# Kernel tuning notes

Measured on AMD Instinct MI355X. Metric: run time of the kernel, lower is better.

## Reference

```python
import jax, jax.numpy as jnp
import numpy as np

N = 100000   # nodes
E = 1200000  # edges
IN, HID, OUT = 64, 64, 64
G = 64       # graphs in the batch


def setup_inputs() -> dict:
    key = jax.random.key(0)
    ks = jax.random.split(key, 7)
    x = jax.random.normal(ks[0], (N, IN), dtype=jnp.float32)
    edge_index = jax.random.randint(ks[1], (2, E), 0, N, dtype=jnp.int32)
    batch = jnp.sort(jax.random.randint(ks[2], (N,), 0, G, dtype=jnp.int32))
    W1 = jax.random.normal(ks[3], (IN, HID), dtype=jnp.float32) * (1.0 / np.sqrt(IN))
    b1 = jnp.zeros((HID,), dtype=jnp.float32)
    W2 = jax.random.normal(ks[4], (HID, OUT), dtype=jnp.float32) * (1.0 / np.sqrt(HID))
    b2 = jnp.zeros((OUT,), dtype=jnp.float32)
    return {"x": x, "edge_index": edge_index, "batch": batch,
            "W1": W1, "b1": b1, "W2": W2, "b2": b2}


def _gcn_conv(x, W, b, src, dst, dinv):
    # x' = D^{-1/2} (A + I) D^{-1/2} (x W) + b   (PyG GCNConv with self-loops)
    h = x @ W                                   # [N, F_out]
    norm = dinv[src] * dinv[dst]                # [E]
    agg = jax.ops.segment_sum(h[src] * norm[:, None], dst, num_segments=N)
    agg = agg + h * (dinv * dinv)[:, None]      # self-loop contribution
    return agg + b


def reference(x, edge_index, batch, W1, b1, W2, b2):
    src, dst = edge_index[0], edge_index[1]
    # degree with self-loops, counted at the aggregation target (PyG convention)
    deg = jax.ops.segment_sum(jnp.ones((E,), x.dtype), dst, num_segments=N) + 1.0
    dinv = jax.lax.rsqrt(deg)

    h1 = jax.nn.relu(_gcn_conv(x, W1, b1, src, dst, dinv))   # [N, HID]
    s1 = jax.ops.segment_sum(h1, batch, num_segments=G)      # [G, HID]
    h2 = jax.nn.relu(_gcn_conv(h1, W2, b2, src, dst, dinv))  # [N, OUT]
    s2 = jax.ops.segment_sum(h2, batch, num_segments=G)      # [G, OUT]
    return h2, jnp.concatenate([s1, s2], axis=1)
```

## Files before the change

kernel.cpp:

```cpp
#include <hip/hip_runtime.h>


#define FDIM 64
#define BSHIFT 7
#define MAXNB 1024
#define EBCAP 2048
#define COLCAP 3072
#define BCAP 4096

__device__ __forceinline__ unsigned short f2bf(float f) {
    union { float f; unsigned int u; } a; a.f = f;
    unsigned int u = a.u;
    unsigned int r = u + 0x7fffu + ((u >> 16) & 1u);
    return (unsigned short)(r >> 16);
}
__device__ __forceinline__ float bf2f(unsigned short s) {
    union { unsigned int u; float f; } a; a.u = ((unsigned int)s) << 16;
    return a.f;
}

__global__ __launch_bounds__(256, 4) void k_pre(
    const int* __restrict__ src, const int* __restrict__ dstp, int E,
    const int* __restrict__ batch, int N, int G, int gemmB, int scatB,
    const float* __restrict__ x, const float* __restrict__ W1,
    int* __restrict__ bucketFill, int* __restrict__ gstart,
    unsigned short* __restrict__ gb1, unsigned int* __restrict__ ebuf) {
    __shared__ __align__(16) char sm[33792];
    int tid = threadIdx.x;
    int bx = blockIdx.x;
    if (bx < gemmB) {
        float4* Ws = (float4*)sm;
        float (*Xs)[68] = (float(*)[68])(sm + 16384);
        ushort4* GB4 = (ushort4*)gb1;
        if (bx == 0 && tid < 16) GB4[(size_t)N * 16 + tid] = make_ushort4(0, 0, 0, 0);
        const float4* W4 = (const float4*)W1;
        for (int i = tid; i < 1024; i += 256) Ws[i] = W4[i];
        int rowBase = bx * 64;
        for (int i = tid; i < 1024; i += 256) {
            int r = i >> 4, f4 = i & 15;
            float4 v = make_float4(0.f, 0.f, 0.f, 0.f);
            if (rowBase + r < N) v = ((const float4*)x)[(size_t)(rowBase + r) * 16 + f4];
            *(float4*)&Xs[r][f4 * 4] = v;
        }
        __syncthreads();
        int r0 = (tid >> 4) * 4;
        int c4 = tid & 15;
        float4 acc0 = make_float4(0,0,0,0), acc1 = acc0, acc2 = acc0, acc3 = acc0;
#pragma unroll 16
        for (int k = 0; k < 64; k++) {
            float4 w = Ws[k * 16 + c4];
            float x0 = Xs[r0 + 0][k], x1 = Xs[r0 + 1][k], x2 = Xs[r0 + 2][k], x3 = Xs[r0 + 3][k];
            acc0.x += x0 * w.x; acc0.y += x0 * w.y; acc0.z += x0 * w.z; acc0.w += x0 * w.w;
            acc1.x += x1 * w.x; acc1.y += x1 * w.y; acc1.z += x1 * w.z; acc1.w += x1 * w.w;
            acc2.x += x2 * w.x; acc2.y += x2 * w.y; acc2.z += x2 * w.z; acc2.w += x2 * w.w;
            acc3.x += x3 * w.x; acc3.y += x3 * w.y; acc3.z += x3 * w.z; acc3.w += x3 * w.w;
        }
        float4 a[4] = {acc0, acc1, acc2, acc3};
#pragma unroll
        for (int i = 0; i < 4; i++) {
            int row = rowBase + r0 + i;
            if (row < N) {
                ushort4 pk;
                pk.x = f2bf(a[i].x); pk.y = f2bf(a[i].y);
                pk.z = f2bf(a[i].z); pk.w = f2bf(a[i].w);
                GB4[(size_t)row * 16 + c4] = pk;
            }
        }
        return;
    }
    if (bx < gemmB + scatB) {
        int* hist = (int*)sm;
        int* base = hist + MAXNB;
        for (int i = tid; i < MAXNB; i += 256) hist[i] = 0;
        __syncthreads();
        int e0 = (bx - gemmB) * 4096;
        int s[16], d[16], r[16];
#pragma unroll
        for (int k = 0; k < 16; k++) {
            int e = e0 + k * 256 + tid;
            bool valid = e < E;
            s[k] = valid ? src[e] : 0;
            d[k] = valid ? dstp[e] : 0;
            r[k] = valid ? atomicAdd(&hist[d[k] >> BSHIFT], 1) : 0;
        }
        __syncthreads();
        for (int i = tid; i < MAXNB; i += 256) {
            int c = hist[i];
            base[i] = c ? (i << 11) + atomicAdd(&bucketFill[i], c) : 0;
        }
        __syncthreads();
#pragma unroll
        for (int k = 0; k < 16; k++) {
            int e = e0 + k * 256 + tid;
            if (e < E)
                ebuf[base[d[k] >> BSHIFT] + r[k]] =
                    (unsigned int)s[k] | ((unsigned int)(d[k] & 127) << 17);
        }
        return;
    }
    int i = (bx - gemmB - scatB) * 256 + tid;
    if (i < N) {
        int b = batch[i];
        if (i == 0) { for (int g = 0; g <= b; g++) gstart[g] = 0; }
        else {
            int pp = batch[i - 1];
            for (int g = pp + 1; g <= b; g++) gstart[g] = i;
        }
        if (i == N - 1) { for (int g = b + 1; g <= G; g++) gstart[g] = N; }
    }
}

__global__ __launch_bounds__(256) void k_bsort(const unsigned int* __restrict__ ebuf,
                                               const int* __restrict__ bucketFill, int N,
                                               int* __restrict__ row_ptr,
                                               int* __restrict__ row_blocks,
                                               int* __restrict__ col,
                                               float* __restrict__ dinv,
                                               unsigned short* __restrict__ gb1) {
    __shared__ int cntL[128];
    __shared__ int scanL[128];
    __shared__ int fillL[128];
    __shared__ int colL[BCAP];
    __shared__ int padT;
    int b = blockIdx.x;
    int n0 = b << BSHIFT;
    int nCnt = N - n0; if (nCnt > 128) nCnt = 128;
    int t = threadIdx.x;
    if (b == 0 && t == 0) dinv[N] = 0.f;
    int cnt = bucketFill[b]; if (cnt > EBCAP) cnt = EBCAP;
    int lo = b << 11, hi = lo + cnt;
    int outBase = b * COLCAP;
    if (t < 128) { cntL[t] = 0; fillL[t] = 0; }
    __syncthreads();
    for (int e = lo + t; e < hi; e += 256)
        atomicAdd(&cntL[ebuf[e] >> 17], 1);
    __syncthreads();
    int pc = 0;
    if (t < 128) { pc = (cntL[t] + 7) & ~7; scanL[t] = pc; }
    __syncthreads();
    for (int off = 1; off < 128; off <<= 1) {
        int u = (t >= off && t < 128) ? scanL[t - off] : 0;
        __syncthreads();
        if (t < 128) scanL[t] += u;
        __syncthreads();
    }
    if (t == 127) padT = scanL[127];
    if (t < nCnt) {
        int ex = scanL[t] - pc;
        row_ptr[n0 + t] = outBase + ex;
        row_blocks[n0 + t] = pc >> 3;
        dinv[n0 + t] = rsqrtf((float)cntL[t] + 1.0f);
        scanL[t] = ex;
    }
    __syncthreads();
    int padTotal = padT;
    if (padTotal <= BCAP) {
        for (int i = t; i < padTotal; i += 256) colL[i] = N;
        __syncthreads();
        for (int e = lo + t; e < hi; e += 256) {
            unsigned int pr = ebuf[e];
            int d = pr >> 17;
            int r = scanL[d] + atomicAdd(&fillL[d], 1);
            colL[r] = (int)(pr & 0x1FFFFu);
        }
        __syncthreads();
        for (int i = t; i < padTotal; i += 256) col[outBase + i] = colL[i];
    } else {
        for (int e = lo + t; e < hi; e += 256) {
            unsigned int pr = ebuf[e];
            int d = pr >> 17;
            int r = scanL[d] + atomicAdd(&fillL[d], 1);
            col[outBase + r] = (int)(pr & 0x1FFFFu);
        }
        __syncthreads();
        if (t < nCnt) {
            int pcl = (cntL[t] + 7) & ~7;
            for (int i = cntL[t]; i < pcl; i++) col[outBase + scanL[t] + i] = N;
        }
    }
    __syncthreads();
    ushort4* GB4 = (ushort4*)gb1;
    for (int i = t; i < nCnt * 16; i += 256) {
        int row = i >> 4, u4 = i & 15;
        float dn = rsqrtf((float)cntL[row] + 1.0f);
        size_t idx = (size_t)(n0 + row) * 16 + u4;
        ushort4 u = GB4[idx];
        u.x = f2bf(bf2f(u.x) * dn);
        u.y = f2bf(bf2f(u.y) * dn);
        u.z = f2bf(bf2f(u.z) * dn);
        u.w = f2bf(bf2f(u.w) * dn);
        GB4[idx] = u;
    }
}

template <typename OutT>
__global__ __launch_bounds__(256) void k_agg(
    const unsigned short* __restrict__ Gb,
    const int* __restrict__ row_ptr, const int* __restrict__ row_blocks,
    const int* __restrict__ col, const float* __restrict__ dinv,
    const float* __restrict__ bias, int N, OutT* __restrict__ Out) {
    int w = threadIdx.x >> 6;
    int c = threadIdx.x & 63;
    int n = blockIdx.x * 4 + w;
    if (n >= N) return;
    int e = row_ptr[n];
    int nb8 = row_blocks[n];
    float acc = bf2f(Gb[(size_t)n * FDIM + c]);
    for (; nb8 >= 2; nb8 -= 2, e += 16) {
        int4 ca = *(const int4*)(col + e);
        int4 cb = *(const int4*)(col + e + 4);
        int4 cc = *(const int4*)(col + e + 8);
        int4 cd = *(const int4*)(col + e + 12);
        int s0  = __builtin_amdgcn_readfirstlane(ca.x);
        int s1  = __builtin_amdgcn_readfirstlane(ca.y);
        int s2  = __builtin_amdgcn_readfirstlane(ca.z);
        int s3  = __builtin_amdgcn_readfirstlane(ca.w);
        int s4  = __builtin_amdgcn_readfirstlane(cb.x);
        int s5  = __builtin_amdgcn_readfirstlane(cb.y);
        int s6  = __builtin_amdgcn_readfirstlane(cb.z);
        int s7  = __builtin_amdgcn_readfirstlane(cb.w);
        int s8  = __builtin_amdgcn_readfirstlane(cc.x);
        int s9  = __builtin_amdgcn_readfirstlane(cc.y);
        int s10 = __builtin_amdgcn_readfirstlane(cc.z);
        int s11 = __builtin_amdgcn_readfirstlane(cc.w);
        int s12 = __builtin_amdgcn_readfirstlane(cd.x);
        int s13 = __builtin_amdgcn_readfirstlane(cd.y);
        int s14 = __builtin_amdgcn_readfirstlane(cd.z);
        int s15 = __builtin_amdgcn_readfirstlane(cd.w);
        float a0  = bf2f(Gb[(size_t)s0  * FDIM + c]);
        float a1  = bf2f(Gb[(size_t)s1  * FDIM + c]);
        float a2  = bf2f(Gb[(size_t)s2  * FDIM + c]);
        float a3  = bf2f(Gb[(size_t)s3  * FDIM + c]);
        float a4  = bf2f(Gb[(size_t)s4  * FDIM + c]);
        float a5  = bf2f(Gb[(size_t)s5  * FDIM + c]);
        float a6  = bf2f(Gb[(size_t)s6  * FDIM + c]);
        float a7  = bf2f(Gb[(size_t)s7  * FDIM + c]);
        float a8  = bf2f(Gb[(size_t)s8  * FDIM + c]);
        float a9  = bf2f(Gb[(size_t)s9  * FDIM + c]);
        float a10 = bf2f(Gb[(size_t)s10 * FDIM + c]);
        float a11 = bf2f(Gb[(size_t)s11 * FDIM + c]);
        float a12 = bf2f(Gb[(size_t)s12 * FDIM + c]);
        float a13 = bf2f(Gb[(size_t)s13 * FDIM + c]);
        float a14 = bf2f(Gb[(size_t)s14 * FDIM + c]);
        float a15 = bf2f(Gb[(size_t)s15 * FDIM + c]);
        acc += (((a0 + a1) + (a2 + a3)) + ((a4 + a5) + (a6 + a7)))
             + (((a8 + a9) + (a10 + a11)) + ((a12 + a13) + (a14 + a15)));
    }
    if (nb8) {
        int4 ca = *(const int4*)(col + e);
        int4 cb = *(const int4*)(col + e + 4);
        int s0 = __builtin_amdgcn_readfirstlane(ca.x);
        int s1 = __builtin_amdgcn_readfirstlane(ca.y);
        int s2 = __builtin_amdgcn_readfirstlane(ca.z);
        int s3 = __builtin_amdgcn_readfirstlane(ca.w);
        int s4 = __builtin_amdgcn_readfirstlane(cb.x);
        int s5 = __builtin_amdgcn_readfirstlane(cb.y);
        int s6 = __builtin_amdgcn_readfirstlane(cb.z);
        int s7 = __builtin_amdgcn_readfirstlane(cb.w);
        float a0 = bf2f(Gb[(size_t)s0 * FDIM + c]);
        float a1 = bf2f(Gb[(size_t)s1 * FDIM + c]);
        float a2 = bf2f(Gb[(size_t)s2 * FDIM + c]);
        float a3 = bf2f(Gb[(size_t)s3 * FDIM + c]);
        float a4 = bf2f(Gb[(size_t)s4 * FDIM + c]);
        float a5 = bf2f(Gb[(size_t)s5 * FDIM + c]);
        float a6 = bf2f(Gb[(size_t)s6 * FDIM + c]);
        float a7 = bf2f(Gb[(size_t)s7 * FDIM + c]);
        acc += ((a0 + a1) + (a2 + a3)) + ((a4 + a5) + (a6 + a7));
    }
    float v = fmaxf(acc * dinv[n] + bias[c], 0.f);
    if constexpr (sizeof(OutT) == 2)
        Out[(size_t)n * FDIM + c] = f2bf(v);
    else
        Out[(size_t)n * FDIM + c] = v;
}

__global__ __launch_bounds__(256, 4) void k_gemm2(
    const unsigned short* __restrict__ H1b, const float* __restrict__ W2,
    const float* __restrict__ dinv, int N, unsigned short* __restrict__ Gb2) {
    __shared__ float4 Ws[64 * 16];
    __shared__ float Xs[64][68];
    int tid = threadIdx.x;
    ushort4* GB4 = (ushort4*)Gb2;
    if (blockIdx.x == 0 && tid < 16)
        GB4[(size_t)N * 16 + tid] = make_ushort4(0, 0, 0, 0);
    const float4* W4 = (const float4*)W2;
    for (int i = tid; i < 1024; i += 256) Ws[i] = W4[i];
    int rowBase = blockIdx.x * 64;
    const ushort4* H4 = (const ushort4*)H1b;
    for (int i = tid; i < 1024; i += 256) {
        int r = i >> 4, u4 = i & 15;
        float4 v = make_float4(0.f, 0.f, 0.f, 0.f);
        if (rowBase + r < N) {
            ushort4 u = H4[(size_t)(rowBase + r) * 16 + u4];
            v = make_float4(bf2f(u.x), bf2f(u.y), bf2f(u.z), bf2f(u.w));
        }
        *(float4*)&Xs[r][u4 * 4] = v;
    }
    __syncthreads();
    int r0 = (tid >> 4) * 4;
    int c4 = tid & 15;
    float4 acc0 = make_float4(0,0,0,0), acc1 = acc0, acc2 = acc0, acc3 = acc0;
#pragma unroll 16
    for (int k = 0; k < 64; k++) {
        float4 w = Ws[k * 16 + c4];
        float x0 = Xs[r0 + 0][k], x1 = Xs[r0 + 1][k], x2 = Xs[r0 + 2][k], x3 = Xs[r0 + 3][k];
        acc0.x += x0 * w.x; acc0.y += x0 * w.y; acc0.z += x0 * w.z; acc0.w += x0 * w.w;
        acc1.x += x1 * w.x; acc1.y += x1 * w.y; acc1.z += x1 * w.z; acc1.w += x1 * w.w;
        acc2.x += x2 * w.x; acc2.y += x2 * w.y; acc2.z += x2 * w.z; acc2.w += x2 * w.w;
        acc3.x += x3 * w.x; acc3.y += x3 * w.y; acc3.z += x3 * w.z; acc3.w += x3 * w.w;
    }
    float4 a[4] = {acc0, acc1, acc2, acc3};
#pragma unroll
    for (int i = 0; i < 4; i++) {
        int row = rowBase + r0 + i;
        if (row < N) {
            float dn = dinv[row];
            ushort4 pk;
            pk.x = f2bf(a[i].x * dn);
            pk.y = f2bf(a[i].y * dn);
            pk.z = f2bf(a[i].z * dn);
            pk.w = f2bf(a[i].w * dn);
            GB4[(size_t)row * 16 + c4] = pk;
        }
    }
}

__global__ __launch_bounds__(256) void k_pool(const unsigned short* __restrict__ H1b,
                                              const float4* __restrict__ H2,
                                              const int* __restrict__ gstart,
                                              float* __restrict__ pool) {
    int g = blockIdx.x & 63;
    int layer = blockIdx.x >> 6;
    int lo = gstart[g], hi = gstart[g + 1];
    int c4 = threadIdx.x & 15;
    int rl = threadIdx.x >> 4;
    float4 acc = make_float4(0.f, 0.f, 0.f, 0.f);
    if (layer == 0) {
        const ushort4* H = (const ushort4*)H1b;
        for (int r = lo + rl; r < hi; r += 16) {
            ushort4 u = H[(size_t)r * 16 + c4];
            acc.x += bf2f(u.x); acc.y += bf2f(u.y);
            acc.z += bf2f(u.z); acc.w += bf2f(u.w);
        }
    } else {
        for (int r = lo + rl; r < hi; r += 16) {
            float4 v = H2[(size_t)r * 16 + c4];
            acc.x += v.x; acc.y += v.y; acc.z += v.z; acc.w += v.w;
        }
    }
    __shared__ float4 sm[16][16];
    sm[rl][c4] = acc;
    __syncthreads();
    if (rl == 0) {
        float4 s = sm[0][c4];
#pragma unroll
        for (int k = 1; k < 16; k++) {
            float4 v = sm[k][c4];
            s.x += v.x; s.y += v.y; s.z += v.z; s.w += v.w;
        }
        float* dstq = &pool[(size_t)g * 128 + layer * 64 + c4 * 4];
        dstq[0] = s.x; dstq[1] = s.y; dstq[2] = s.z; dstq[3] = s.w;
    }
}

static inline size_t align256(size_t x) { return (x + 255) & ~(size_t)255; }

extern "C" void kernel_launch(void* const* d_in, const int* in_sizes, int n_in,
                              void* d_out, int out_size, void* d_ws, size_t ws_size,
                              hipStream_t stream) {
    const float* x     = (const float*)d_in[0];
    const int*   ei    = (const int*)d_in[1];
    const int*   batch = (const int*)d_in[2];
    const float* W1    = (const float*)d_in[3];
    const float* b1    = (const float*)d_in[4];
    const float* W2    = (const float*)d_in[5];
    const float* b2    = (const float*)d_in[6];

    const int N = in_sizes[0] / FDIM;
    const int E = in_sizes[1] / 2;
    const int G = 64;
    const int NB = (N + 127) >> BSHIFT;
    const int* src = ei;
    const int* dst = ei + E;

    char* p = (char*)d_ws;
    int* row_ptr     = (int*)p; p += align256(((size_t)N + 1) * 4);
    int* row_blocks  = (int*)p; p += align256((size_t)N * 4);
    int* col         = (int*)p; p += align256((size_t)NB * COLCAP * 4);
    int* bucketFill  = (int*)p; p += align256((size_t)MAXNB * 4);
    int* gstart      = (int*)p; p += align256((size_t)(G + 1) * 4);
    float* dinv      = (float*)p; p += align256(((size_t)N + 1) * 4);
    unsigned short* gb1 = (unsigned short*)p; p += align256(((size_t)N + 1) * FDIM * 2);
    unsigned short* gb2 = (unsigned short*)p; p += align256(((size_t)N + 1) * FDIM * 2);
    unsigned short* h1b = (unsigned short*)p; p += align256((size_t)N * FDIM * 2);
    unsigned int* ebuf = (unsigned int*)h1b;

    float* out  = (float*)d_out;
    float* h2   = out;
    float* pool = out + (size_t)N * FDIM;

    hipMemsetAsync(bucketFill, 0, (size_t)MAXNB * 4, stream);

    int nbB   = (N + 255) / 256;
    int gemmB = (N + 63) / 64;
    int aggB  = (N + 3) / 4;
    int scatB = (E + 4095) / 4096;

    k_pre<<<gemmB + scatB + nbB, 256, 0, stream>>>(src, dst, E, batch, N, G,
                                                   gemmB, scatB, x, W1,
                                                   bucketFill, gstart, gb1, ebuf);
    k_bsort<<<NB, 256, 0, stream>>>(ebuf, bucketFill, N, row_ptr, row_blocks,
                                    col, dinv, gb1);
    k_agg<unsigned short><<<aggB, 256, 0, stream>>>(gb1, row_ptr, row_blocks, col,
                                                    dinv, b1, N, h1b);
    k_gemm2<<<gemmB, 256, 0, stream>>>(h1b, W2, dinv, N, gb2);
    k_agg<float><<<aggB, 256, 0, stream>>>(gb2, row_ptr, row_blocks, col,
                                           dinv, b2, N, h2);
    k_pool<<<2 * G, 256, 0, stream>>>(h1b, (const float4*)h2, gstart, pool);
}
```

Measured before the change: 245.8 us.

## Fuse graph pooling into gemm2 and layer-2 aggregation, drop k_pool kernel

Result: slower. 881.2 us (+258.4%).

```diff
diff --git a/kernel.cpp b/kernel.cpp
--- a/kernel.cpp
+++ b/kernel.cpp
@@ -193,12 +193,11 @@
     }
 }
 
-template <typename OutT>
-__global__ __launch_bounds__(256) void k_agg(
+__global__ __launch_bounds__(256) void k_agg1(
     const unsigned short* __restrict__ Gb,
     const int* __restrict__ row_ptr, const int* __restrict__ row_blocks,
     const int* __restrict__ col, const float* __restrict__ dinv,
-    const float* __restrict__ bias, int N, OutT* __restrict__ Out) {
+    const float* __restrict__ bias, int N, unsigned short* __restrict__ Out) {
     int w = threadIdx.x >> 6;
     int c = threadIdx.x & 63;
     int n = blockIdx.x * 4 + w;
@@ -268,24 +267,56 @@
         acc += ((a0 + a1) + (a2 + a3)) + ((a4 + a5) + (a6 + a7));
     }
     float v = fmaxf(acc * dinv[n] + bias[c], 0.f);
-    if constexpr (sizeof(OutT) == 2)
-        Out[(size_t)n * FDIM + c] = f2bf(v);
-    else
-        Out[(size_t)n * FDIM + c] = v;
+    Out[(size_t)n * FDIM + c] = f2bf(v);
 }
 
 __global__ __launch_bounds__(256, 4) void k_gemm2(
     const unsigned short* __restrict__ H1b, const float* __restrict__ W2,
-    const float* __restrict__ dinv, int N, unsigned short* __restrict__ Gb2) {
-    __shared__ float4 Ws[64 * 16];
-    __shared__ float Xs[64][68];
+    const float* __restrict__ dinv, int N, int gemmB,
+    const int* __restrict__ gstart, float* __restrict__ pool,
+    unsigned short* __restrict__ Gb2) {
+    __shared__ __align__(16) char sm[33792];
     int tid = threadIdx.x;
+    int bx = blockIdx.x;
+    if (bx >= gemmB) {
+        int g = bx - gemmB;
+        int lo = gstart[g], hi = gstart[g + 1];
+        int c4 = tid & 15;
+        int rl = tid >> 4;
+        float4 acc = make_float4(0.f, 0.f, 0.f, 0.f);
+        const ushort4* H = (const ushort4*)H1b;
+        for (int r = lo + rl; r < hi; r += 16) {
+            ushort4 u = H[(size_t)r * 16 + c4];
+            acc.x += bf2f(u.x); acc.y += bf2f(u.y);
+            acc.z += bf2f(u.z); acc.w += bf2f(u.w);
+        }
+        float4 (*smp)[16] = (float4(*)[16])sm;
+        smp[rl][c4] = acc;
+        __syncthreads();
+        if (rl == 0) {
+            float4 s = smp[0][c4];
+#pragma unroll
+            for (int k = 1; k < 16; k++) {
+                float4 v = smp[k][c4];
+                s.x += v.x; s.y += v.y; s.z += v.z; s.w += v.w;
+            }
+            float* dq = &pool[(size_t)g * 128 + c4 * 4];
+            dq[0] = s.x; dq[1] = s.y; dq[2] = s.z; dq[3] = s.w;
+            if (lo == hi) {
+                float* dq2 = dq + 64;
+                dq2[0] = 0.f; dq2[1] = 0.f; dq2[2] = 0.f; dq2[3] = 0.f;
+            }
+        }
+        return;
+    }
+    float4* Ws = (float4*)sm;
+    float (*Xs)[68] = (float(*)[68])(sm + 16384);
     ushort4* GB4 = (ushort4*)Gb2;
-    if (blockIdx.x == 0 && tid < 16)
+    if (bx == 0 && tid < 16)
         GB4[(size_t)N * 16 + tid] = make_ushort4(0, 0, 0, 0);
     const float4* W4 = (const float4*)W2;
     for (int i = tid; i < 1024; i += 256) Ws[i] = W4[i];
-    int rowBase = blockIdx.x * 64;
+    int rowBase = bx * 64;
     const ushort4* H4 = (const ushort4*)H1b;
     for (int i = tid; i < 1024; i += 256) {
         int r = i >> 4, u4 = i & 15;
@@ -325,41 +356,127 @@
     }
 }
 
-__global__ __launch_bounds__(256) void k_pool(const unsigned short* __restrict__ H1b,
-                                              const float4* __restrict__ H2,
-                                              const int* __restrict__ gstart,
-                                              float* __restrict__ pool) {
-    int g = blockIdx.x & 63;
-    int layer = blockIdx.x >> 6;
-    int lo = gstart[g], hi = gstart[g + 1];
-    int c4 = threadIdx.x & 15;
-    int rl = threadIdx.x >> 4;
-    float4 acc = make_float4(0.f, 0.f, 0.f, 0.f);
-    if (layer == 0) {
-        const ushort4* H = (const ushort4*)H1b;
-        for (int r = lo + rl; r < hi; r += 16) {
-            ushort4 u = H[(size_t)r * 16 + c4];
-            acc.x += bf2f(u.x); acc.y += bf2f(u.y);
-            acc.z += bf2f(u.z); acc.w += bf2f(u.w);
-        }
-    } else {
-        for (int r = lo + rl; r < hi; r += 16) {
-            float4 v = H2[(size_t)r * 16 + c4];
-            acc.x += v.x; acc.y += v.y; acc.z += v.z; acc.w += v.w;
-        }
-    }
-    __shared__ float4 sm[16][16];
-    sm[rl][c4] = acc;
-    __syncthreads();
-    if (rl == 0) {
-        float4 s = sm[0][c4];
-#pragma unroll
-        for (int k = 1; k < 16; k++) {
-            float4 v = sm[k][c4];
-            s.x += v.x; s.y += v.y; s.z += v.z; s.w += v.w;
-        }
-        float* dstq = &pool[(size_t)g * 128 + layer * 64 + c4 * 4];
-        dstq[0] = s.x; dstq[1] = s.y; dstq[2] = s.z; dstq[3] = s.w;
+__global__ __launch_bounds__(256) void k_agg2(
+    const unsigned short* __restrict__ Gb,
+    const int* __restrict__ row_ptr, const int* __restrict__ row_blocks,
+    const int* __restrict__ col, const float* __restrict__ dinv,
+    const float* __restrict__ bias, const int* __restrict__ batch,
+    const int* __restrict__ gstart, int* __restrict__ gdone, int N,
+    float* __restrict__ Out, float* __restrict__ pool) {
+    __shared__ int gid[4];
+    __shared__ int pooled[4];
+    __shared__ float pacc[4][64];
+    int w = threadIdx.x >> 6;
+    int c = threadIdx.x & 63;
+    int n = blockIdx.x * 4 + w;
+    if ((threadIdx.x & 63) == 0) gid[w] = (n < N) ? batch[n] : -1;
+    if (n < N) {
+        int e = row_ptr[n];
+        int nb8 = row_blocks[n];
+        float acc = bf2f(Gb[(size_t)n * FDIM + c]);
+        for (; nb8 >= 2; nb8 -= 2, e += 16) {
+            int4 ca = *(const int4*)(col + e);
+            int4 cb = *(const int4*)(col + e + 4);
+            int4 cc = *(const int4*)(col + e + 8);
+            int4 cd = *(const int4*)(col + e + 12);
+            int s0  = __builtin_amdgcn_readfirstlane(ca.x);
+            int s1  = __builtin_amdgcn_readfirstlane(ca.y);
+            int s2  = __builtin_amdgcn_readfirstlane(ca.z);
+            int s3  = __builtin_amdgcn_readfirstlane(ca.w);
+            int s4  = __builtin_amdgcn_readfirstlane(cb.x);
+            int s5  = __builtin_amdgcn_readfirstlane(cb.y);
+            int s6  = __builtin_amdgcn_readfirstlane(cb.z);
+            int s7  = __builtin_amdgcn_readfirstlane(cb.w);
+            int s8  = __builtin_amdgcn_readfirstlane(cc.x);
+            int s9  = __builtin_amdgcn_readfirstlane(cc.y);
+            int s10 = __builtin_amdgcn_readfirstlane(cc.z);
+            int s11 = __builtin_amdgcn_readfirstlane(cc.w);
+            int s12 = __builtin_amdgcn_readfirstlane(cd.x);
+            int s13 = __builtin_amdgcn_readfirstlane(cd.y);
+            int s14 = __builtin_amdgcn_readfirstlane(cd.z);
+            int s15 = __builtin_amdgcn_readfirstlane(cd.w);
+            float a0  = bf2f(Gb[(size_t)s0  * FDIM + c]);
+            float a1  = bf2f(Gb[(size_t)s1  * FDIM + c]);
+            float a2  = bf2f(Gb[(size_t)s2  * FDIM + c]);
+            float a3  = bf2f(Gb[(size_t)s3  * FDIM + c]);
+            float a4  = bf2f(Gb[(size_t)s4  * FDIM + c]);
+            float a5  = bf2f(Gb[(size_t)s5  * FDIM + c]);
+            float a6  = bf2f(Gb[(size_t)s6  * FDIM + c]);
+            float a7  = bf2f(Gb[(size_t)s7  * FDIM + c]);
+            float a8  = bf2f(Gb[(size_t)s8  * FDIM + c]);
+            float a9  = bf2f(Gb[(size_t)s9  * FDIM + c]);
+            float a10 = bf2f(Gb[(size_t)s10 * FDIM + c]);
+            float a11 = bf2f(Gb[(size_t)s11 * FDIM + c]);
+            float a12 = bf2f(Gb[(size_t)s12 * FDIM + c]);
+            float a13 = bf2f(Gb[(size_t)s13 * FDIM + c]);
+            float a14 = bf2f(Gb[(size_t)s14 * FDIM + c]);
+            float a15 = bf2f(Gb[(size_t)s15 * FDIM + c]);
+            acc += (((a0 + a1) + (a2 + a3)) + ((a4 + a5) + (a6 + a7)))
+                 + (((a8 + a9) + (a10 + a11)) + ((a12 + a13) + (a14 + a15)));
+        }
+        if (nb8) {
+            int4 ca = *(const int4*)(col + e);
+            int4 cb = *(const int4*)(col + e + 4);
+            int s0 = __builtin_amdgcn_readfirstlane(ca.x);
+            int s1 = __builtin_amdgcn_readfirstlane(ca.y);
+            int s2 = __builtin_amdgcn_readfirstlane(ca.z);
+            int s3 = __builtin_amdgcn_readfirstlane(ca.w);
+            int s4 = __builtin_amdgcn_readfirstlane(cb.x);
+            int s5 = __builtin_amdgcn_readfirstlane(cb.y);
+            int s6 = __builtin_amdgcn_readfirstlane(cb.z);
+            int s7 = __builtin_amdgcn_readfirstlane(cb.w);
+            float a0 = bf2f(Gb[(size_t)s0 * FDIM + c]);
+            float a1 = bf2f(Gb[(size_t)s1 * FDIM + c]);
+            float a2 = bf2f(Gb[(size_t)s2 * FDIM + c]);
+            float a3 = bf2f(Gb[(size_t)s3 * FDIM + c]);
+            float a4 = bf2f(Gb[(size_t)s4 * FDIM + c]);
+            float a5 = bf2f(Gb[(size_t)s5 * FDIM + c]);
+            float a6 = bf2f(Gb[(size_t)s6 * FDIM + c]);
+            float a7 = bf2f(Gb[(size_t)s7 * FDIM + c]);
+            acc += ((a0 + a1) + (a2 + a3)) + ((a4 + a5) + (a6 + a7));
+        }
+        float v = fmaxf(acc * dinv[n] + bias[c], 0.f);
+        __hip_atomic_store(&Out[(size_t)n * FDIM + c], v,
+                           __ATOMIC_RELAXED, __HIP_MEMORY_SCOPE_AGENT);
+    }
+    __syncthreads();
+    if (threadIdx.x == 0) {
+        int done[4]; done[0] = done[1] = done[2] = done[3] = -1;
+#pragma unroll
+        for (int j = 0; j < 4; j++) pooled[j] = -1;
+        for (int j = 0; j < 4; j++) {
+            int g = gid[j];
+            if (g < 0) continue;
+            bool dup = false;
+            for (int k = 0; k < j; k++) if (gid[k] == g) dup = true;
+            if (dup) continue;
+            int cntg = 0;
+            for (int k = j; k < 4; k++) if (gid[k] == g) cntg++;
+            int old = __hip_atomic_fetch_add(&gdone[g], cntg,
+                                             __ATOMIC_RELEASE, __HIP_MEMORY_SCOPE_AGENT);
+            int gsize = gstart[g + 1] - gstart[g];
+            if (old + cntg == gsize) done[j] = g;
+        }
+#pragma unroll
+        for (int j = 0; j < 4; j++) pooled[j] = done[j];
+    }
+    __syncthreads();
+    for (int j = 0; j < 4; j++) {
+        int g = pooled[j];
+        if (g < 0) continue;
+        int lo = gstart[g], hi = gstart[g + 1];
+        int rl = threadIdx.x >> 6;
+        float acc = 0.f;
+        for (int r = lo + rl; r < hi; r += 4)
+            acc += __hip_atomic_load(&Out[(size_t)r * FDIM + c],
+                                     __ATOMIC_RELAXED, __HIP_MEMORY_SCOPE_AGENT);
+        pacc[rl][c] = acc;
+        __syncthreads();
+        if (rl == 0) {
+            float s = pacc[0][c] + pacc[1][c] + pacc[2][c] + pacc[3][c];
+            pool[(size_t)g * 128 + 64 + c] = s;
+        }
+        __syncthreads();
     }
 }
 
@@ -387,7 +504,8 @@
     int* row_ptr     = (int*)p; p += align256(((size_t)N + 1) * 4);
     int* row_blocks  = (int*)p; p += align256((size_t)N * 4);
     int* col         = (int*)p; p += align256((size_t)NB * COLCAP * 4);
-    int* bucketFill  = (int*)p; p += align256((size_t)MAXNB * 4);
+    int* bucketFill  = (int*)p; p += align256(((size_t)MAXNB + 64) * 4);
+    int* gdone       = bucketFill + MAXNB;
     int* gstart      = (int*)p; p += align256((size_t)(G + 1) * 4);
     float* dinv      = (float*)p; p += align256(((size_t)N + 1) * 4);
     unsigned short* gb1 = (unsigned short*)p; p += align256(((size_t)N + 1) * FDIM * 2);
@@ -399,7 +517,7 @@
     float* h2   = out;
     float* pool = out + (size_t)N * FDIM;
 
-    hipMemsetAsync(bucketFill, 0, (size_t)MAXNB * 4, stream);
+    hipMemsetAsync(bucketFill, 0, ((size_t)MAXNB + 64) * 4, stream);
 
     int nbB   = (N + 255) / 256;
     int gemmB = (N + 63) / 64;
@@ -411,10 +529,8 @@
                                                    bucketFill, gstart, gb1, ebuf);
     k_bsort<<<NB, 256, 0, stream>>>(ebuf, bucketFill, N, row_ptr, row_blocks,
                                     col, dinv, gb1);
-    k_agg<unsigned short><<<aggB, 256, 0, stream>>>(gb1, row_ptr, row_blocks, col,
-                                                    dinv, b1, N, h1b);
-    k_gemm2<<<gemmB, 256, 0, stream>>>(h1b, W2, dinv, N, gb2);
-    k_agg<float><<<aggB, 256, 0, stream>>>(gb2, row_ptr, row_blocks, col,
-                                           dinv, b2, N, h2);
-    k_pool<<<2 * G, 256, 0, stream>>>(h1b, (const float4*)h2, gstart, pool);
-}
+    k_agg1<<<aggB, 256, 0, stream>>>(gb1, row_ptr, row_blocks, col, dinv, b1, N, h1b);
+    k_gemm2<<<gemmB + G, 256, 0, stream>>>(h1b, W2, dinv, N, gemmB, gstart, pool, gb2);
+    k_agg2<<<aggB, 256, 0, stream>>>(gb2, row_ptr, row_blocks, col, dinv, b2,
+                                     batch, gstart, gdone, N, h2, pool);
+}
```
